# Kernel optimization log

Measured on AMD Instinct MI355X. Metric: run time of the kernel, lower is better.

## Reference

```python
import jax, jax.numpy as jnp
import numpy as np
from jax import lax

HIDDEN = 1024
STATE = 64
BATCH = 16
SEQ = 2048
DT_MIN, DT_MAX = 0.001, 0.1


def setup_inputs() -> dict:
    key = jax.random.key(0)
    k = jax.random.split(key, 6)
    x = jax.random.normal(k[0], (BATCH, SEQ, HIDDEN), dtype=jnp.float32)
    A = jax.random.normal(k[1], (STATE, STATE), dtype=jnp.float32) * 0.01
    B = jax.random.normal(k[2], (STATE, HIDDEN), dtype=jnp.float32) * 0.01
    C = jax.random.normal(k[3], (HIDDEN, STATE), dtype=jnp.float32) * 0.01
    D = jnp.ones((HIDDEN,), dtype=jnp.float32)
    log_dt = jax.random.uniform(k[4], (HIDDEN,), dtype=jnp.float32) * (
        np.log(DT_MAX) - np.log(DT_MIN)
    ) + np.log(DT_MIN)
    return {"x": x, "A": A, "B": B, "C": C, "D": D, "log_dt": log_dt}


def reference(x, A, B, C, D, log_dt):
    # x: (B, T, H)
    dt = jnp.exp(log_dt)                                  # (H,)
    A_bar = jax.scipy.linalg.expm(A * dt.mean())          # (N, N)
    B_bar = B * dt[None, :]                               # (N, H)
    # Precompute input injection for all timesteps: (B, T, N)
    u = jnp.einsum("bth,nh->btn", x, B_bar)

    def step(state, u_t):
        # state: (B, N); u_t: (B, N)
        state = state @ A_bar.T + u_t
        return state, state

    init = jnp.zeros((x.shape[0], A.shape[0]), dtype=x.dtype)
    _, states = lax.scan(step, init, jnp.swapaxes(u, 0, 1))  # (T, B, N)
    states = jnp.swapaxes(states, 0, 1)                      # (B, T, N)
    return jnp.einsum("btn,hn->bth", states, C) + D * x
```

## Files before the change

kernel.cpp:

```cpp
#include <hip/hip_runtime.h>


#define H   1024
#define NS  64
#define NB  16
#define TT  2048
#define LCH 64
#define KCH 32

typedef __attribute__((ext_vector_type(8))) short bf16x8;
typedef __attribute__((ext_vector_type(4))) float f32x4;
typedef __attribute__((ext_vector_type(2))) unsigned int u32x2;

#define WS_ABAR 0
#define WS_AL   4096
#define WS_F    8192
#define WS_P    40960
#define WS_U    73728
#define WS_S    2170880

__device__ __forceinline__ unsigned short f2bf(float x) {
  union { float f; unsigned u; } v; v.f = x;
  unsigned r = (v.u + 0x7FFFu + ((v.u >> 16) & 1u)) >> 16;
  return (unsigned short)r;
}

__device__ __forceinline__ bf16x8 packbf8(f32x4 a, f32x4 b) {
  bf16x8 r;
  r[0] = (short)f2bf(a[0]); r[1] = (short)f2bf(a[1]);
  r[2] = (short)f2bf(a[2]); r[3] = (short)f2bf(a[3]);
  r[4] = (short)f2bf(b[0]); r[5] = (short)f2bf(b[1]);
  r[6] = (short)f2bf(b[2]); r[7] = (short)f2bf(b[3]);
  return r;
}

__device__ __forceinline__ u32x2 packbf4(f32x4 v) {
  u32x2 r;
  r[0] = (unsigned)f2bf(v[0]) | ((unsigned)f2bf(v[1]) << 16);
  r[1] = (unsigned)f2bf(v[2]) | ((unsigned)f2bf(v[3]) << 16);
  return r;
}

__device__ __forceinline__ f32x4 mfma16(bf16x8 a, bf16x8 b, f32x4 c) {
  return __builtin_amdgcn_mfma_f32_16x16x32_bf16(a, b, c, 0, 0, 0);
}

__device__ void prep_block(const float* Ain, const float* ldt, float* ws, int which) {
  __shared__ float Mb[64 * 68];
  __shared__ short Tl[64 * 72];
  const int lane = threadIdx.x;
  const int cq = lane >> 4, cl = lane & 15;

  float s = 0.f;
  for (int j = 0; j < 16; ++j) s += expf(ldt[lane + j * 64]);
  for (int off = 32; off; off >>= 1) s += __shfl_down(s, off);
  float dtm = __shfl(s, 0) * (1.0f / 1024.0f);
  float scale = which ? dtm * (float)LCH : dtm;

  for (int idx = lane; idx < 4096; idx += 64) {
    int r = idx >> 6, c = idx & 63;
    float v = Ain[idx] * scale;
    Mb[c * 68 + r] = v;
    Tl[r * 72 + c] = (short)f2bf(v);
  }

  float E[16][4];
  for (int mt = 0; mt < 4; ++mt)
    for (int nt = 0; nt < 4; ++nt)
      for (int r = 0; r < 4; ++r) {
        int row = mt * 16 + cq * 4 + r, col = nt * 16 + cl;
        E[mt * 4 + nt][r] = (row == col ? 1.f : 0.f) + Ain[row * 64 + col] * scale;
      }

  __asm volatile("s_waitcnt lgkmcnt(0)" ::: "memory");

  for (int it = 2; it <= 12; ++it) {
    bf16x8 af[4][2];
    for (int mt = 0; mt < 4; ++mt)
      for (int kh = 0; kh < 2; ++kh)
        af[mt][kh] = *(const bf16x8*)&Tl[(mt * 16 + cl) * 72 + kh * 32 + cq * 8];
    float inv = 1.0f / (float)it;
    bf16x8 bfr[4][2];
    for (int nt = 0; nt < 4; ++nt)
      for (int kh = 0; kh < 2; ++kh) {
        const float* p = &Mb[(nt * 16 + cl) * 68 + kh * 32 + cq * 8];
        f32x4 a = *(const f32x4*)p;
        f32x4 b = *(const f32x4*)(p + 4);
        bfr[nt][kh] = packbf8(a * inv, b * inv);
      }
    f32x4 zero = {0.f, 0.f, 0.f, 0.f};
    f32x4 acc[16];
    for (int i = 0; i < 16; ++i) acc[i] = zero;
    for (int mt = 0; mt < 4; ++mt)
      for (int nt = 0; nt < 4; ++nt) {
        acc[mt * 4 + nt] = mfma16(af[mt][0], bfr[nt][0], acc[mt * 4 + nt]);
        acc[mt * 4 + nt] = mfma16(af[mt][1], bfr[nt][1], acc[mt * 4 + nt]);
      }
    __asm volatile("s_waitcnt lgkmcnt(0)" ::: "memory");
    for (int mt = 0; mt < 4; ++mt)
      for (int nt = 0; nt < 4; ++nt)
        for (int r = 0; r < 4; ++r) {
          float t = acc[mt * 4 + nt][r];
          E[mt * 4 + nt][r] += t;
          Tl[(mt * 16 + cq * 4 + r) * 72 + nt * 16 + cl] = (short)f2bf(t);
        }
    __asm volatile("s_waitcnt lgkmcnt(0)" ::: "memory");
  }

  float* dst = ws + (which ? WS_AL : WS_ABAR);
  for (int mt = 0; mt < 4; ++mt)
    for (int nt = 0; nt < 4; ++nt)
      for (int r = 0; r < 4; ++r)
        dst[(mt * 16 + cq * 4 + r) * 64 + nt * 16 + cl] = E[mt * 4 + nt][r];
}

__device__ void gemm_u(const float* x, const float* Bm, const float* ldt, float* u2, int bid) {
  __shared__ short xl[64 * 40];
  __shared__ short bl[64 * 40];
  const int tid = threadIdx.x;
  const int bt0 = bid * 64;
  const int wid = tid >> 6, lane = tid & 63;
  const int cq = lane >> 4, cl = lane & 15;
  const int mst = tid >> 2, k0 = (tid & 3) * 8;

  f32x4 zero = {0.f, 0.f, 0.f, 0.f};
  f32x4 acc[4];
  for (int i = 0; i < 4; ++i) acc[i] = zero;

  const float* xrow = x + (long)(bt0 + mst) * H + k0;
  const float* brow = Bm + (long)mst * H + k0;

  for (int hc = 0; hc < 32; ++hc) {
    int h0 = hc * 32;
    f32x4 xa = *(const f32x4*)(xrow + h0);
    f32x4 xb = *(const f32x4*)(xrow + h0 + 4);
    f32x4 ba = *(const f32x4*)(brow + h0);
    f32x4 bb = *(const f32x4*)(brow + h0 + 4);
    f32x4 da, db;
    for (int j = 0; j < 4; ++j) {
      da[j] = expf(ldt[h0 + k0 + j]);
      db[j] = expf(ldt[h0 + k0 + 4 + j]);
    }
    *(bf16x8*)&xl[mst * 40 + k0] = packbf8(xa, xb);
    *(bf16x8*)&bl[mst * 40 + k0] = packbf8(ba * da, bb * db);
    __syncthreads();
    bf16x8 afr = *(const bf16x8*)&xl[(wid * 16 + cl) * 40 + cq * 8];
    for (int nt = 0; nt < 4; ++nt) {
      bf16x8 bfr = *(const bf16x8*)&bl[(nt * 16 + cl) * 40 + cq * 8];
      acc[nt] = mfma16(afr, bfr, acc[nt]);
    }
    __syncthreads();
  }
  for (int nt = 0; nt < 4; ++nt)
    for (int r = 0; r < 4; ++r) {
      int bt = bt0 + wid * 16 + cq * 4 + r;
      int t = bt & (TT - 1), b = bt >> 11;
      u2[(long)(t * 16 + b) * 64 + nt * 16 + cl] = acc[nt][r];
    }
}

__global__ __launch_bounds__(256) void k1(const float* x, const float* Ain, const float* Bm,
                                          const float* ldt, float* ws) {
  if (blockIdx.x < 2) {
    if (threadIdx.x < 64) prep_block(Ain, ldt, ws, blockIdx.x);
    return;
  }
  gemm_u(x, Bm, ldt, ws + WS_U, blockIdx.x - 2);
}

__device__ __forceinline__ void load_RF(const float* Amat, bf16x8 Rf[4][2], int cq, int cl) {
  for (int mt = 0; mt < 4; ++mt)
    for (int kh = 0; kh < 2; ++kh) {
      int m = mt * 16 + cl;
      int kb = kh * 32 + cq * 8;
      f32x4 v0 = *(const f32x4*)&Amat[m * 64 + kb];
      f32x4 v1 = *(const f32x4*)&Amat[m * 64 + kb + 4];
      for (int j = 0; j < 4; ++j) {
        if (m == kb + j) v0[j] -= 1.f;
        if (m == kb + 4 + j) v1[j] -= 1.f;
      }
      Rf[mt][kh] = packbf8(v0, v1);
    }
}

__device__ __forceinline__ void scan_step(f32x4 Z[4], const bf16x8 Rf[4][2], short* Zl,
                                          const f32x4 U[4], int cq, int cl) {
  for (int t = 0; t < 4; ++t)
    *(u32x2*)&Zl[cl * 72 + t * 16 + cq * 4] = packbf4(Z[t]);
  __asm volatile("s_waitcnt lgkmcnt(0)" ::: "memory");
  bf16x8 zf0 = *(const bf16x8*)&Zl[cl * 72 + cq * 8];
  bf16x8 zf1 = *(const bf16x8*)&Zl[cl * 72 + 32 + cq * 8];
  for (int t = 0; t < 4; ++t) Z[t] += U[t];
  for (int mt = 0; mt < 4; ++mt) {
    Z[mt] = mfma16(Rf[mt][0], zf0, Z[mt]);
    Z[mt] = mfma16(Rf[mt][1], zf1, Z[mt]);
  }
}

__global__ __launch_bounds__(64) void scan_local_k(float* ws) {
  const float* Abar = ws + WS_ABAR;
  const float* u2 = ws + WS_U;
  float* F = ws + WS_F;
  __shared__ short Zl[16 * 72];
  const int lane = threadIdx.x, cq = lane >> 4, cl = lane & 15;
  const int c = blockIdx.x;
  bf16x8 Rf[4][2];
  load_RF(Abar, Rf, cq, cl);
  f32x4 zero = {0.f, 0.f, 0.f, 0.f};
  f32x4 Z[4], U[4], Un[4];
  for (int t = 0; t < 4; ++t) Z[t] = zero;
  const float* ub = u2 + (long)c * LCH * 1024 + cl * 64 + cq * 4;
  for (int t = 0; t < 4; ++t) U[t] = *(const f32x4*)(ub + t * 16);
  for (int ti = 0; ti < LCH; ++ti) {
    const float* un = ub + (ti + 1) * 1024;
    for (int t = 0; t < 4; ++t) Un[t] = *(const f32x4*)(un + t * 16);
    scan_step(Z, Rf, Zl, U, cq, cl);
    for (int t = 0; t < 4; ++t) U[t] = Un[t];
  }
  for (int t = 0; t < 4; ++t)
    *(f32x4*)&F[(long)c * 1024 + cl * 64 + t * 16 + cq * 4] = Z[t];
}

__global__ __launch_bounds__(64) void scan_chunks_k(float* ws) {
  const float* AL = ws + WS_AL;
  const float* F = ws + WS_F;
  float* P = ws + WS_P;
  __shared__ short Zl[16 * 72];
  const int lane = threadIdx.x, cq = lane >> 4, cl = lane & 15;
  bf16x8 Rf[4][2];
  load_RF(AL, Rf, cq, cl);
  f32x4 zero = {0.f, 0.f, 0.f, 0.f};
  f32x4 Z[4], U[4];
  for (int t = 0; t < 4; ++t) Z[t] = zero;
  for (int c = 0; c < KCH; ++c) {
    long off = (long)c * 1024 + cl * 64 + cq * 4;
    for (int t = 0; t < 4; ++t) *(f32x4*)&P[off + t * 16] = Z[t];
    for (int t = 0; t < 4; ++t) U[t] = *(const f32x4*)&F[off + t * 16];
    scan_step(Z, Rf, Zl, U, cq, cl);
  }
}

__global__ __launch_bounds__(64) void scan_final_k(float* ws) {
  const float* Abar = ws + WS_ABAR;
  const float* u2 = ws + WS_U;
  const float* P = ws + WS_P;
  float* S2 = ws + WS_S;
  __shared__ short Zl[16 * 72];
  const int lane = threadIdx.x, cq = lane >> 4, cl = lane & 15;
  const int c = blockIdx.x;
  bf16x8 Rf[4][2];
  load_RF(Abar, Rf, cq, cl);
  f32x4 Z[4], U[4], Un[4];
  long poff = (long)c * 1024 + cl * 64 + cq * 4;
  for (int t = 0; t < 4; ++t) Z[t] = *(const f32x4*)&P[poff + t * 16];
  const float* ub = u2 + (long)c * LCH * 1024 + cl * 64 + cq * 4;
  float* sb = S2 + (long)c * LCH * 1024 + cl * 64 + cq * 4;
  for (int t = 0; t < 4; ++t) U[t] = *(const f32x4*)(ub + t * 16);
  for (int ti = 0; ti < LCH; ++ti) {
    const float* un = ub + (ti + 1) * 1024;
    for (int t = 0; t < 4; ++t) Un[t] = *(const f32x4*)(un + t * 16);
    scan_step(Z, Rf, Zl, U, cq, cl);
    float* so = sb + ti * 1024;
    for (int t = 0; t < 4; ++t) *(f32x4*)(so + t * 16) = Z[t];
    for (int t = 0; t < 4; ++t) U[t] = Un[t];
  }
}

__global__ __launch_bounds__(256) void out_proj_k(const float* ws, const float* Cm,
                                                  const float* Dv, const float* x, float* out) {
  const float* S2 = ws + WS_S;
  __shared__ short sl[64 * 72];
  __shared__ short cls[128 * 72];
  const int tid = threadIdx.x;
  const int bid = blockIdx.x;
  const int bt0 = (bid & 511) * 64;
  const int h0 = (bid >> 9) * 128;
  const int wid = tid >> 6, lane = tid & 63;
  const int cq = lane >> 4, cl = lane & 15;

  {
    int m = tid >> 2, k0 = (tid & 3) * 16;
    int bt = bt0 + m, t = bt & (TT - 1), b = bt >> 11;
    const float* sr = S2 + (long)(t * 16 + b) * 64 + k0;
    f32x4 a0 = *(const f32x4*)(sr);
    f32x4 a1 = *(const f32x4*)(sr + 4);
    f32x4 a2 = *(const f32x4*)(sr + 8);
    f32x4 a3 = *(const f32x4*)(sr + 12);
    *(bf16x8*)&sl[m * 72 + k0] = packbf8(a0, a1);
    *(bf16x8*)&sl[m * 72 + k0 + 8] = packbf8(a2, a3);

    int hl = tid >> 1, kc = (tid & 1) * 32;
    const float* cr = Cm + (long)(h0 + hl) * 64 + kc;
    f32x4 c0 = *(const f32x4*)(cr);
    f32x4 c1 = *(const f32x4*)(cr + 4);
    f32x4 c2 = *(const f32x4*)(cr + 8);
    f32x4 c3 = *(const f32x4*)(cr + 12);
    f32x4 c4 = *(const f32x4*)(cr + 16);
    f32x4 c5 = *(const f32x4*)(cr + 20);
    f32x4 c6 = *(const f32x4*)(cr + 24);
    f32x4 c7 = *(const f32x4*)(cr + 28);
    *(bf16x8*)&cls[hl * 72 + kc] = packbf8(c0, c1);
    *(bf16x8*)&cls[hl * 72 + kc + 8] = packbf8(c2, c3);
    *(bf16x8*)&cls[hl * 72 + kc + 16] = packbf8(c4, c5);
    *(bf16x8*)&cls[hl * 72 + kc + 24] = packbf8(c6, c7);
  }
  __syncthreads();

  bf16x8 af0 = *(const bf16x8*)&sl[(wid * 16 + cl) * 72 + cq * 8];
  bf16x8 af1 = *(const bf16x8*)&sl[(wid * 16 + cl) * 72 + 32 + cq * 8];
  f32x4 zero = {0.f, 0.f, 0.f, 0.f};
  for (int nt = 0; nt < 8; ++nt) {
    bf16x8 b0 = *(const bf16x8*)&cls[(nt * 16 + cl) * 72 + cq * 8];
    bf16x8 b1 = *(const bf16x8*)&cls[(nt * 16 + cl) * 72 + 32 + cq * 8];
    f32x4 acc = zero;
    acc = mfma16(af0, b0, acc);
    acc = mfma16(af1, b1, acc);
    int h = h0 + nt * 16 + cl;
    float d = Dv[h];
    for (int r = 0; r < 4; ++r) {
      long bt = bt0 + wid * 16 + cq * 4 + r;
      long idx = bt * H + h;
      out[idx] = acc[r] + d * x[idx];
    }
  }
}

extern "C" void kernel_launch(void* const* d_in, const int* in_sizes, int n_in,
                              void* d_out, int out_size, void* d_ws, size_t ws_size,
                              hipStream_t stream) {
  const float* x = (const float*)d_in[0];
  const float* A = (const float*)d_in[1];
  const float* Bm = (const float*)d_in[2];
  const float* Cm = (const float*)d_in[3];
  const float* Dv = (const float*)d_in[4];
  const float* ldt = (const float*)d_in[5];
  float* out = (float*)d_out;
  float* ws = (float*)d_ws;

  k1<<<dim3(2 + 512), dim3(256), 0, stream>>>(x, A, Bm, ldt, ws);
  scan_local_k<<<dim3(KCH), dim3(64), 0, stream>>>(ws);
  scan_chunks_k<<<dim3(1), dim3(64), 0, stream>>>(ws);
  scan_final_k<<<dim3(KCH), dim3(64), 0, stream>>>(ws);
  out_proj_k<<<dim3(4096), dim3(256), 0, stream>>>(ws, Cm, Dv, x, out);
}
```

Measured before the change: 541.9 us.

## Pre-swizzle B and C weights into MFMA fragment layout, rebalance scan chunks

Adds a prep kernel that converts dt-scaled B and C to bf16 and stores them in MFMA fragment order. The input and output projection kernels can then load fragments straight from global memory without LDS staging or __syncthreads. Scan chunks change from 32×64 to 64×32, giving the two local-scan passes more parallel blocks and shorter serial chains while lengthening the cross-chunk scan. Input prefetch in the scans deepens to two steps, and the output projection covers 256 columns per block in a (t,b)-major row order. Costs are an extra kernel launch and a longer single-block chunk scan.

After: 551.5 us. About the same (+1.8%).

```diff
diff --git a/kernel.cpp b/kernel.cpp
--- a/kernel.cpp
+++ b/kernel.cpp
@@ -5,8 +5,8 @@
 #define NS  64
 #define NB  16
 #define TT  2048
-#define LCH 64
-#define KCH 32
+#define LCH 32
+#define KCH 64
 
 typedef __attribute__((ext_vector_type(8))) short bf16x8;
 typedef __attribute__((ext_vector_type(4))) float f32x4;
@@ -14,10 +14,12 @@
 
 #define WS_ABAR 0
 #define WS_AL   4096
-#define WS_F    8192
-#define WS_P    40960
-#define WS_U    73728
-#define WS_S    2170880
+#define WS_WF   8192
+#define WS_CF   40960
+#define WS_F    73728
+#define WS_P    139264
+#define WS_U    204800
+#define WS_S    2301952
 
 __device__ __forceinline__ unsigned short f2bf(float x) {
   union { float f; unsigned u; } v; v.f = x;
@@ -114,58 +116,66 @@
         dst[(mt * 16 + cq * 4 + r) * 64 + nt * 16 + cl] = E[mt * 4 + nt][r];
 }
 
-__device__ void gemm_u(const float* x, const float* Bm, const float* ldt, float* u2, int bid) {
-  __shared__ short xl[64 * 40];
-  __shared__ short bl[64 * 40];
+__global__ __launch_bounds__(256) void prep_k(const float* Ain, const float* Bm,
+                                              const float* Cm, const float* ldt, float* ws) {
+  const int bid = blockIdx.x;
+  if (bid < 2) {
+    if (threadIdx.x < 64) prep_block(Ain, ldt, ws, bid);
+    return;
+  }
+  if (bid < 10) {
+    unsigned short* wf = (unsigned short*)(ws + WS_WF);
+    int tg = (bid - 2) * 256 + threadIdx.x;
+    int f0 = tg * 32;
+    for (int i = 0; i < 32; ++i) {
+      int f = f0 + i;
+      int j = f & 7, cl = (f >> 3) & 15, quad = (f >> 7) & 3, nt = (f >> 9) & 3, hc = f >> 11;
+      int n = nt * 16 + cl, h = hc * 32 + quad * 8 + j;
+      wf[f] = f2bf(Bm[n * 1024 + h] * expf(ldt[h]));
+    }
+  } else {
+    unsigned short* cf = (unsigned short*)(ws + WS_CF);
+    int tg = (bid - 10) * 256 + threadIdx.x;
+    int f0 = tg * 32;
+    for (int i = 0; i < 32; ++i) {
+      int f = f0 + i;
+      int j = f & 7, cl = (f >> 3) & 15, quad = (f >> 7) & 3, kc = (f >> 9) & 1, ht = f >> 10;
+      int h = ht * 16 + cl, n = kc * 32 + quad * 8 + j;
+      cf[f] = f2bf(Cm[h * 64 + n]);
+    }
+  }
+}
+
+__global__ __launch_bounds__(256) void gemm_u_k(const float* x, float* ws) {
+  const unsigned short* wf = (const unsigned short*)(ws + WS_WF);
+  float* u2 = ws + WS_U;
   const int tid = threadIdx.x;
-  const int bt0 = bid * 64;
   const int wid = tid >> 6, lane = tid & 63;
-  const int cq = lane >> 4, cl = lane & 15;
-  const int mst = tid >> 2, k0 = (tid & 3) * 8;
-
+  const int quad = lane >> 4, cl = lane & 15;
+  const int mt = blockIdx.x * 4 + wid;
+  const int bt0w = mt * 16;
+
+  const float* xrow = x + (long)(bt0w + cl) * H + quad * 8;
   f32x4 zero = {0.f, 0.f, 0.f, 0.f};
   f32x4 acc[4];
   for (int i = 0; i < 4; ++i) acc[i] = zero;
 
-  const float* xrow = x + (long)(bt0 + mst) * H + k0;
-  const float* brow = Bm + (long)mst * H + k0;
-
+#pragma unroll 4
   for (int hc = 0; hc < 32; ++hc) {
-    int h0 = hc * 32;
-    f32x4 xa = *(const f32x4*)(xrow + h0);
-    f32x4 xb = *(const f32x4*)(xrow + h0 + 4);
-    f32x4 ba = *(const f32x4*)(brow + h0);
-    f32x4 bb = *(const f32x4*)(brow + h0 + 4);
-    f32x4 da, db;
-    for (int j = 0; j < 4; ++j) {
-      da[j] = expf(ldt[h0 + k0 + j]);
-      db[j] = expf(ldt[h0 + k0 + 4 + j]);
-    }
-    *(bf16x8*)&xl[mst * 40 + k0] = packbf8(xa, xb);
-    *(bf16x8*)&bl[mst * 40 + k0] = packbf8(ba * da, bb * db);
-    __syncthreads();
-    bf16x8 afr = *(const bf16x8*)&xl[(wid * 16 + cl) * 40 + cq * 8];
+    f32x4 xa = *(const f32x4*)(xrow + hc * 32);
+    f32x4 xb = *(const f32x4*)(xrow + hc * 32 + 4);
+    bf16x8 af = packbf8(xa, xb);
     for (int nt = 0; nt < 4; ++nt) {
-      bf16x8 bfr = *(const bf16x8*)&bl[(nt * 16 + cl) * 40 + cq * 8];
-      acc[nt] = mfma16(afr, bfr, acc[nt]);
-    }
-    __syncthreads();
+      bf16x8 bfr = *(const bf16x8*)&wf[((hc * 16 + nt * 4 + quad) * 16 + cl) * 8];
+      acc[nt] = mfma16(af, bfr, acc[nt]);
+    }
   }
   for (int nt = 0; nt < 4; ++nt)
     for (int r = 0; r < 4; ++r) {
-      int bt = bt0 + wid * 16 + cq * 4 + r;
-      int t = bt & (TT - 1), b = bt >> 11;
+      int g = bt0w + quad * 4 + r;
+      int t = g & (TT - 1), b = g >> 11;
       u2[(long)(t * 16 + b) * 64 + nt * 16 + cl] = acc[nt][r];
     }
-}
-
-__global__ __launch_bounds__(256) void k1(const float* x, const float* Ain, const float* Bm,
-                                          const float* ldt, float* ws) {
-  if (blockIdx.x < 2) {
-    if (threadIdx.x < 64) prep_block(Ain, ldt, ws, blockIdx.x);
-    return;
-  }
-  gemm_u(x, Bm, ldt, ws + WS_U, blockIdx.x - 2);
 }
 
 __device__ __forceinline__ void load_RF(const float* Amat, bf16x8 Rf[4][2], int cq, int cl) {
@@ -207,15 +217,16 @@
   bf16x8 Rf[4][2];
   load_RF(Abar, Rf, cq, cl);
   f32x4 zero = {0.f, 0.f, 0.f, 0.f};
-  f32x4 Z[4], U[4], Un[4];
+  f32x4 Z[4], U0[4], U1[4], Un[4];
   for (int t = 0; t < 4; ++t) Z[t] = zero;
   const float* ub = u2 + (long)c * LCH * 1024 + cl * 64 + cq * 4;
-  for (int t = 0; t < 4; ++t) U[t] = *(const f32x4*)(ub + t * 16);
+  for (int t = 0; t < 4; ++t) U0[t] = *(const f32x4*)(ub + t * 16);
+  for (int t = 0; t < 4; ++t) U1[t] = *(const f32x4*)(ub + 1024 + t * 16);
   for (int ti = 0; ti < LCH; ++ti) {
-    const float* un = ub + (ti + 1) * 1024;
+    const float* un = ub + (ti + 2) * 1024;
     for (int t = 0; t < 4; ++t) Un[t] = *(const f32x4*)(un + t * 16);
-    scan_step(Z, Rf, Zl, U, cq, cl);
-    for (int t = 0; t < 4; ++t) U[t] = Un[t];
+    scan_step(Z, Rf, Zl, U0, cq, cl);
+    for (int t = 0; t < 4; ++t) { U0[t] = U1[t]; U1[t] = Un[t]; }
   }
   for (int t = 0; t < 4; ++t)
     *(f32x4*)&F[(long)c * 1024 + cl * 64 + t * 16 + cq * 4] = Z[t];
@@ -230,13 +241,18 @@
   bf16x8 Rf[4][2];
   load_RF(AL, Rf, cq, cl);
   f32x4 zero = {0.f, 0.f, 0.f, 0.f};
-  f32x4 Z[4], U[4];
+  f32x4 Z[4], U0[4], U1[4], Un[4];
   for (int t = 0; t < 4; ++t) Z[t] = zero;
+  const float* fb = F + cl * 64 + cq * 4;
+  for (int t = 0; t < 4; ++t) U0[t] = *(const f32x4*)(fb + t * 16);
+  for (int t = 0; t < 4; ++t) U1[t] = *(const f32x4*)(fb + 1024 + t * 16);
   for (int c = 0; c < KCH; ++c) {
     long off = (long)c * 1024 + cl * 64 + cq * 4;
     for (int t = 0; t < 4; ++t) *(f32x4*)&P[off + t * 16] = Z[t];
-    for (int t = 0; t < 4; ++t) U[t] = *(const f32x4*)&F[off + t * 16];
-    scan_step(Z, Rf, Zl, U, cq, cl);
+    const float* fn = fb + (c + 2) * 1024;
+    for (int t = 0; t < 4; ++t) Un[t] = *(const f32x4*)(fn + t * 16);
+    scan_step(Z, Rf, Zl, U0, cq, cl);
+    for (int t = 0; t < 4; ++t) { U0[t] = U1[t]; U1[t] = Un[t]; }
   }
 }
 
@@ -250,76 +266,58 @@
   const int c = blockIdx.x;
   bf16x8 Rf[4][2];
   load_RF(Abar, Rf, cq, cl);
-  f32x4 Z[4], U[4], Un[4];
+  f32x4 Z[4], U0[4], U1[4], Un[4];
   long poff = (long)c * 1024 + cl * 64 + cq * 4;
   for (int t = 0; t < 4; ++t) Z[t] = *(const f32x4*)&P[poff + t * 16];
   const float* ub = u2 + (long)c * LCH * 1024 + cl * 64 + cq * 4;
   float* sb = S2 + (long)c * LCH * 1024 + cl * 64 + cq * 4;
-  for (int t = 0; t < 4; ++t) U[t] = *(const f32x4*)(ub + t * 16);
+  for (int t = 0; t < 4; ++t) U0[t] = *(const f32x4*)(ub + t * 16);
+  for (int t = 0; t < 4; ++t) U1[t] = *(const f32x4*)(ub + 1024 + t * 16);
   for (int ti = 0; ti < LCH; ++ti) {
-    const float* un = ub + (ti + 1) * 1024;
+    const float* un = ub + (ti + 2) * 1024;
     for (int t = 0; t < 4; ++t) Un[t] = *(const f32x4*)(un + t * 16);
-    scan_step(Z, Rf, Zl, U, cq, cl);
+    scan_step(Z, Rf, Zl, U0, cq, cl);
     float* so = sb + ti * 1024;
     for (int t = 0; t < 4; ++t) *(f32x4*)(so + t * 16) = Z[t];
-    for (int t = 0; t < 4; ++t) U[t] = Un[t];
-  }
-}
-
-__global__ __launch_bounds__(256) void out_proj_k(const float* ws, const float* Cm,
-                                                  const float* Dv, const float* x, float* out) {
+    for (int t = 0; t < 4; ++t) { U0[t] = U1[t]; U1[t] = Un[t]; }
+  }
+}
+
+__global__ __launch_bounds__(256) void out_proj_k(const float* ws, const float* Dv,
+                                                  const float* x, float* out) {
   const float* S2 = ws + WS_S;
-  __shared__ short sl[64 * 72];
-  __shared__ short cls[128 * 72];
+  const unsigned short* cf = (const unsigned short*)(ws + WS_CF);
   const int tid = threadIdx.x;
   const int bid = blockIdx.x;
-  const int bt0 = (bid & 511) * 64;
-  const int h0 = (bid >> 9) * 128;
+  const int rg = bid & 511, hg = bid >> 9;
   const int wid = tid >> 6, lane = tid & 63;
-  const int cq = lane >> 4, cl = lane & 15;
-
-  {
-    int m = tid >> 2, k0 = (tid & 3) * 16;
-    int bt = bt0 + m, t = bt & (TT - 1), b = bt >> 11;
-    const float* sr = S2 + (long)(t * 16 + b) * 64 + k0;
-    f32x4 a0 = *(const f32x4*)(sr);
-    f32x4 a1 = *(const f32x4*)(sr + 4);
-    f32x4 a2 = *(const f32x4*)(sr + 8);
-    f32x4 a3 = *(const f32x4*)(sr + 12);
-    *(bf16x8*)&sl[m * 72 + k0] = packbf8(a0, a1);
-    *(bf16x8*)&sl[m * 72 + k0 + 8] = packbf8(a2, a3);
-
-    int hl = tid >> 1, kc = (tid & 1) * 32;
-    const float* cr = Cm + (long)(h0 + hl) * 64 + kc;
-    f32x4 c0 = *(const f32x4*)(cr);
-    f32x4 c1 = *(const f32x4*)(cr + 4);
-    f32x4 c2 = *(const f32x4*)(cr + 8);
-    f32x4 c3 = *(const f32x4*)(cr + 12);
-    f32x4 c4 = *(const f32x4*)(cr + 16);
-    f32x4 c5 = *(const f32x4*)(cr + 20);
-    f32x4 c6 = *(const f32x4*)(cr + 24);
-    f32x4 c7 = *(const f32x4*)(cr + 28);
-    *(bf16x8*)&cls[hl * 72 + kc] = packbf8(c0, c1);
-    *(bf16x8*)&cls[hl * 72 + kc + 8] = packbf8(c2, c3);
-    *(bf16x8*)&cls[hl * 72 + kc + 16] = packbf8(c4, c5);
-    *(bf16x8*)&cls[hl * 72 + kc + 24] = packbf8(c6, c7);
-  }
-  __syncthreads();
-
-  bf16x8 af0 = *(const bf16x8*)&sl[(wid * 16 + cl) * 72 + cq * 8];
-  bf16x8 af1 = *(const bf16x8*)&sl[(wid * 16 + cl) * 72 + 32 + cq * 8];
+  const int quad = lane >> 4, cl = lane & 15;
+  const int mt = rg * 4 + wid;
+  const int s0 = mt * 16;
+  const int h0 = hg * 256;
+
+  const float* sr = S2 + (long)(s0 + cl) * 64 + quad * 8;
+  f32x4 a00 = *(const f32x4*)(sr);
+  f32x4 a01 = *(const f32x4*)(sr + 4);
+  f32x4 a10 = *(const f32x4*)(sr + 32);
+  f32x4 a11 = *(const f32x4*)(sr + 36);
+  bf16x8 af0 = packbf8(a00, a01);
+  bf16x8 af1 = packbf8(a10, a11);
+
   f32x4 zero = {0.f, 0.f, 0.f, 0.f};
-  for (int nt = 0; nt < 8; ++nt) {
-    bf16x8 b0 = *(const bf16x8*)&cls[(nt * 16 + cl) * 72 + cq * 8];
-    bf16x8 b1 = *(const bf16x8*)&cls[(nt * 16 + cl) * 72 + 32 + cq * 8];
+  const int t = mt;
+  for (int nt = 0; nt < 16; ++nt) {
+    int htg = (h0 >> 4) + nt;
+    bf16x8 b0 = *(const bf16x8*)&cf[(((htg * 2 + 0) * 4 + quad) * 16 + cl) * 8];
+    bf16x8 b1 = *(const bf16x8*)&cf[(((htg * 2 + 1) * 4 + quad) * 16 + cl) * 8];
     f32x4 acc = zero;
     acc = mfma16(af0, b0, acc);
     acc = mfma16(af1, b1, acc);
     int h = h0 + nt * 16 + cl;
     float d = Dv[h];
     for (int r = 0; r < 4; ++r) {
-      long bt = bt0 + wid * 16 + cq * 4 + r;
-      long idx = bt * H + h;
+      int b = quad * 4 + r;
+      long idx = ((long)b * TT + t) * H + h;
       out[idx] = acc[r] + d * x[idx];
     }
   }
@@ -337,9 +335,10 @@
   float* out = (float*)d_out;
   float* ws = (float*)d_ws;
 
-  k1<<<dim3(2 + 512), dim3(256), 0, stream>>>(x, A, Bm, ldt, ws);
+  prep_k<<<dim3(18), dim3(256), 0, stream>>>(A, Bm, Cm, ldt, ws);
+  gemm_u_k<<<dim3(512), dim3(256), 0, stream>>>(x, ws);
   scan_local_k<<<dim3(KCH), dim3(64), 0, stream>>>(ws);
   scan_chunks_k<<<dim3(1), dim3(64), 0, stream>>>(ws);
   scan_final_k<<<dim3(KCH), dim3(64), 0, stream>>>(ws);
-  out_proj_k<<<dim3(4096), dim3(256), 0, stream>>>(ws, Cm, Dv, x, out);
-}
+  out_proj_k<<<dim3(2048), dim3(256), 0, stream>>>(ws, Dv, x, out);
+}
```
